# Performance work log

Measured on AMD Instinct MI355X. Metric: run time of the kernel, lower is better.

## Reference

```python
import jax, jax.numpy as jnp
import numpy as np
from math import log2

B, N, H, D, HID, BLK = 4, 4096, 16, 64, 1024, 128
THETA = 10000.0
SCALE = D ** -0.5
ATTN_EPS = 1e-8
LN_EPS = 1e-5


def setup_inputs() -> dict:
    key = jax.random.key(0)
    ks = jax.random.split(key, 3)
    return {
        "hidden_states": jax.random.normal(ks[0], (B, N, HID), jnp.float32),
        "ln_gamma": jnp.ones((HID,), jnp.float32),
        "ln_beta": jnp.zeros((HID,), jnp.float32),
        "w_qkv": jax.random.normal(ks[1], (HID, 3 * H * D), jnp.float32) * 0.02,
        "w_out": jax.random.normal(ks[2], (H * D, HID), jnp.float32) * 0.02,
        "b_out": jnp.zeros((HID,), jnp.float32),
    }


def _rotary_freqs(n):
    # faithful to source: 1.0 / (theta ** arange(0,dim,2) / dim)  (note precedence)
    exps = jnp.arange(0, D, 2, dtype=jnp.float32)[: D // 2]
    inv = 1.0 / (THETA ** exps / D)
    f = jnp.arange(n, dtype=jnp.float32)[:, None] * inv[None, :]  # (n, D/2)
    return jnp.repeat(f, 2, axis=-1)  # (n, D), each freq duplicated pairwise


def _apply_rotary(freqs, t):
    cos, sin = jnp.cos(freqs), jnp.sin(freqs)  # (n, D) broadcast over (bh, n, D)
    x = t.reshape(*t.shape[:-1], D // 2, 2)
    rot = jnp.stack((-x[..., 1], x[..., 0]), axis=-1).reshape(t.shape)
    return t * cos + rot * sin


def _flip_pairs(t):
    # flip every adjacent pair along axis 1
    s = t.shape
    t = t.reshape(s[0], s[1] // 2, 2, *s[2:])
    return t[:, :, ::-1].reshape(s)


def _coarsen(q, k, v):
    pair = lambda t: t.reshape(t.shape[0], -1, 2, D)
    return pair(q).mean(2), pair(k).mean(2), pair(v).sum(2)


def _block_attn(q, k, v):
    # q,k,v: (bh, nblk, z, d); unnormalized softmax numerator + denominator
    S = jnp.einsum('bnid,bnjd->bnij', q, k)
    S = S - S.max(-1, keepdims=True)
    A = jnp.exp(S)
    y = jnp.einsum('bnij,bnjd->bnid', A, v)
    return y.reshape(y.shape[0], -1, D), A.sum(-1).reshape(A.shape[0], -1)


def _forward(hidden_states, ln_gamma, ln_beta, w_qkv, w_out, b_out):
    # LayerNorm
    mu = hidden_states.mean(-1, keepdims=True)
    var = hidden_states.var(-1, keepdims=True)
    x = (hidden_states - mu) / jnp.sqrt(var + LN_EPS) * ln_gamma + ln_beta

    # QKV projection, split heads -> (B*H, N, D)
    qkv = x @ w_qkv
    q, k, v = jnp.split(qkv, 3, axis=-1)
    heads = lambda t: t.reshape(B, N, H, D).transpose(0, 2, 1, 3).reshape(B * H, N, D)
    q, k, v = heads(q), heads(k), heads(v)

    q = q * SCALE
    freqs = _rotary_freqs(N)
    q = _apply_rotary(freqs, q)
    k = _apply_rotary(freqs, k)

    num_levels = int(log2(N // BLK)) - 1
    qkvs = [(q, k, v)]
    for _ in range(num_levels):
        qkvs.append(_coarsen(*qkvs[-1]))
    qkvs = [qkvs[0]] + qkvs  # finest level used twice (near + flipped neighbor)

    Ys = []
    n_lv = len(qkvs)
    for ind, (q_, k_, v_) in enumerate(reversed(qkvs)):
        is_last = ind == n_lv - 1
        tb = lambda t: t.reshape(t.shape[0], -1, BLK, D)
        qb, kb, vb = tb(q_), tb(k_), tb(v_)
        if not is_last:
            kb, vb = _flip_pairs(kb), _flip_pairs(vb)
        Ys.append(_block_attn(qb, kb, vb))

    Y, A = Ys[0]
    for ind in range(1, len(Ys)):
        if ind != len(Ys) - 1:
            Y = jnp.repeat(Y, 2, axis=1)
            A = jnp.repeat(A, 2, axis=1)
        Y = Ys[ind][0] + Y
        A = Ys[ind][1] + A

    out = Y / (A + ATTN_EPS)[..., None]
    out = out.reshape(B, H, N, D).transpose(0, 2, 1, 3).reshape(B, N, H * D)
    return out @ w_out + b_out


def reference(hidden_states, ln_gamma, ln_beta, w_qkv, w_out, b_out):
    return _forward(hidden_states, ln_gamma, ln_beta, w_qkv, w_out, b_out)
```

## Files before the change

kernel.cpp:

```cpp
#include <hip/hip_runtime.h>
#include <math.h>

#define NTOK 4096
#define NB 4
#define NH 16
#define HD 64
#define HID 1024
#define BH 64
#define QSCALE 0.125f

typedef unsigned short u16;
typedef unsigned int u32;
typedef __attribute__((ext_vector_type(8))) _Float16 f16x8;
typedef __attribute__((ext_vector_type(8))) short s16x8;
typedef __attribute__((ext_vector_type(4))) float f32x4;
#define MFMA_F16(a, b, c) __builtin_amdgcn_mfma_f32_16x16x32_f16(a, b, c, 0, 0, 0)
#define MFMA_BF16(a, b, c) __builtin_amdgcn_mfma_f32_16x16x32_bf16(a, b, c, 0, 0, 0)
#define GLDS16(gptr, lptr)                                                          \
  __builtin_amdgcn_global_load_lds(                                                \
      (const __attribute__((address_space(1))) void*)(gptr),                       \
      (__attribute__((address_space(3))) void*)(lptr), 16, 0, 0)
#define VMCNT0() asm volatile("s_waitcnt vmcnt(0)" ::: "memory")
#define VMCNT4() asm volatile("s_waitcnt vmcnt(4)" ::: "memory")
#define SCHED_FENCE() __builtin_amdgcn_sched_barrier(0)

__device__ __forceinline__ float bf2f(u32 u) {
  union { u32 i; float f; } x; x.i = u << 16; return x.f;
}
__device__ __forceinline__ u32 f2bf(float f) {
  union { float f; u32 i; } x; x.f = f;
  return (x.i + 0x7fffu + ((x.i >> 16) & 1u)) >> 16;
}
__device__ __forceinline__ u32 pk2(float a, float b) {
  return f2bf(a) | (f2bf(b) << 16);
}
__device__ __forceinline__ u32 pkh2(float a, float b) {
  _Float16 ha = (_Float16)a, hb = (_Float16)b;
  u16 x, y;
  __builtin_memcpy(&x, &ha, 2);
  __builtin_memcpy(&y, &hb, 2);
  return (u32)x | ((u32)y << 16);
}
__device__ __forceinline__ u16 f2h(float a) {
  _Float16 h = (_Float16)a;
  u16 x;
  __builtin_memcpy(&x, &h, 2);
  return x;
}
__device__ __forceinline__ void up8(uint4 a, float* f) {
  f[0] = bf2f(a.x & 0xffffu); f[1] = bf2f(a.x >> 16);
  f[2] = bf2f(a.y & 0xffffu); f[3] = bf2f(a.y >> 16);
  f[4] = bf2f(a.z & 0xffffu); f[5] = bf2f(a.z >> 16);
  f[6] = bf2f(a.w & 0xffffu); f[7] = bf2f(a.w >> 16);
}
__device__ __forceinline__ void up8h(uint4 a, float* f) {
  union { uint4 u; _Float16 h[8]; } x;
  x.u = a;
#pragma unroll
  for (int c = 0; c < 8; ++c) f[c] = (float)x.h[c];
}

__global__ void fill_kernel(float* __restrict__ out, int n, float v) {
  int i = blockIdx.x * 256 + threadIdx.x;
  if (i < n) out[i] = v;
}

__global__ void rope_table_kernel(float* __restrict__ ct, float* __restrict__ st) {
  int idx = blockIdx.x * 256 + threadIdx.x;
  if (idx >= NTOK * 32) return;
  int n = idx >> 5, i = idx & 31;
  float t = powf(10000.0f, (float)(2 * i));
  float inv = 1.0f / (t / 64.0f);
  float f = (float)n * inv;
  ct[idx] = cosf(f);
  st[idx] = sinf(f);
}

__global__ __launch_bounds__(256) void ln_f16_kernel(const float* __restrict__ in,
                                                     const float* __restrict__ gm,
                                                     const float* __restrict__ bt,
                                                     u16* __restrict__ out) {
  __shared__ float sh[8];
  int row = blockIdx.x, t = threadIdx.x;
  float4 x = ((const float4*)(in + (size_t)row * HID))[t];
  float s1 = x.x + x.y + x.z + x.w;
  float s2 = x.x * x.x + x.y * x.y + x.z * x.z + x.w * x.w;
#pragma unroll
  for (int o = 32; o > 0; o >>= 1) {
    s1 += __shfl_down(s1, o, 64);
    s2 += __shfl_down(s2, o, 64);
  }
  if ((t & 63) == 0) { sh[t >> 6] = s1; sh[4 + (t >> 6)] = s2; }
  __syncthreads();
  float S1 = sh[0] + sh[1] + sh[2] + sh[3];
  float S2 = sh[4] + sh[5] + sh[6] + sh[7];
  float mu = S1 * (1.0f / HID);
  float var = S2 * (1.0f / HID) - mu * mu;
  float rstd = 1.0f / sqrtf(var + 1e-5f);
  float4 g = ((const float4*)gm)[t], b = ((const float4*)bt)[t];
  float o0 = (x.x - mu) * rstd * g.x + b.x;
  float o1 = (x.y - mu) * rstd * g.y + b.y;
  float o2 = (x.z - mu) * rstd * g.z + b.z;
  float o3 = (x.w - mu) * rstd * g.w + b.w;
  *(uint2*)&out[(size_t)row * HID + t * 4] = make_uint2(pkh2(o0, o1), pkh2(o2, o3));
}

__global__ __launch_bounds__(256) void prep_w_kernel(const float* __restrict__ w,
                                                     u16* __restrict__ wt, int N) {
  __shared__ float T[64][65];
  int t = threadIdx.x;
  int n0 = blockIdx.x * 64, k0 = blockIdx.y * 64;
  {
    int k = t >> 2, nc = (t & 3) * 16;
    const float* src = w + (size_t)(k0 + k) * N + n0 + nc;
#pragma unroll
    for (int i = 0; i < 4; ++i) {
      float4 x = *(const float4*)(src + i * 4);
      T[nc + i * 4 + 0][k] = x.x;
      T[nc + i * 4 + 1][k] = x.y;
      T[nc + i * 4 + 2][k] = x.z;
      T[nc + i * 4 + 3][k] = x.w;
    }
  }
  __syncthreads();
  {
    int n = t >> 2, kc = (t & 3) * 16;
    u32 pk[8];
#pragma unroll
    for (int j = 0; j < 8; ++j) pk[j] = pkh2(T[n][kc + 2 * j], T[n][kc + 2 * j + 1]);
    size_t dst = (size_t)(n0 + n) * 1024 + k0 + kc;
    *(uint4*)&wt[dst] = make_uint4(pk[0], pk[1], pk[2], pk[3]);
    *(uint4*)&wt[dst + 8] = make_uint4(pk[4], pk[5], pk[6], pk[7]);
  }
}

template <int MODE>
__global__ __launch_bounds__(256) void gemm_f16_kernel(
    const u16* __restrict__ At, const u16* __restrict__ Bt,
    u16* __restrict__ qd, u16* __restrict__ kd, u16* __restrict__ vd,
    const float* __restrict__ ct, const float* __restrict__ st,
    const float* __restrict__ bias, float* __restrict__ C, int nxb) {
  constexpr int BUF = 128 * 32;
  __shared__ __align__(16) u16 As[3 * BUF], Bs[3 * BUF];
  const int t = threadIdx.x;
  const int nwg = gridDim.x;
  const int bid = blockIdx.x;
  const int wid = (bid & 7) * (nwg >> 3) + (bid >> 3);
  const int m0 = (wid / nxb) * 128, n0 = (wid % nxb) * 128;
  const int l = t & 63, w = t >> 6;
  const int wm = w & 1, wn = w >> 1;
  const int lr = l & 15;
  const int kgs = (((l >> 4) ^ ((lr >> 1) & 3))) * 8;

  const int schunk = (l & 3) ^ ((l >> 3) & 3);
  const u16* gA = At + (size_t)(m0 + w * 32 + (l >> 2)) * 1024 + schunk * 8;
  const u16* gB = Bt + (size_t)(n0 + w * 32 + (l >> 2)) * 1024 + schunk * 8;
  const int wbase = (w * 32) * 32;

  f32x4 zero4 = {0.f, 0.f, 0.f, 0.f};
  f32x4 acc[4][4];
#pragma unroll
  for (int mf = 0; mf < 4; ++mf)
#pragma unroll
    for (int nf = 0; nf < 4; ++nf) acc[mf][nf] = zero4;

  GLDS16(gA, &As[wbase]);
  GLDS16(gA + (size_t)16 * 1024, &As[wbase + 16 * 32]);
  GLDS16(gB, &Bs[wbase]);
  GLDS16(gB + (size_t)16 * 1024, &Bs[wbase + 16 * 32]);
  GLDS16(gA + 32, &As[BUF + wbase]);
  GLDS16(gA + 32 + (size_t)16 * 1024, &As[BUF + wbase + 16 * 32]);
  GLDS16(gB + 32, &Bs[BUF + wbase]);
  GLDS16(gB + 32 + (size_t)16 * 1024, &Bs[BUF + wbase + 16 * 32]);
  VMCNT4();
  __builtin_amdgcn_s_barrier();
  SCHED_FENCE();

  int cur = 0;
  for (int step = 0; step < 32; ++step) {
    int nx2 = cur + 2; if (nx2 >= 3) nx2 -= 3;
    if (step + 2 < 32) {
      int k2 = (step + 2) * 32;
      GLDS16(gA + k2, &As[nx2 * BUF + wbase]);
      GLDS16(gA + k2 + (size_t)16 * 1024, &As[nx2 * BUF + wbase + 16 * 32]);
      GLDS16(gB + k2, &Bs[nx2 * BUF + wbase]);
      GLDS16(gB + k2 + (size_t)16 * 1024, &Bs[nx2 * BUF + wbase + 16 * 32]);
    }
    {
      const int cb = cur * BUF;
      f16x8 af[4];
#pragma unroll
      for (int mf = 0; mf < 4; ++mf)
        af[mf] = *(const f16x8*)&As[cb + (wm * 64 + mf * 16 + lr) * 32 + kgs];
#pragma unroll
      for (int nf = 0; nf < 4; ++nf) {
        f16x8 bf = *(const f16x8*)&Bs[cb + (wn * 64 + nf * 16 + lr) * 32 + kgs];
#pragma unroll
        for (int mf = 0; mf < 4; ++mf) acc[mf][nf] = MFMA_F16(af[mf], bf, acc[mf][nf]);
      }
    }
    if (step + 1 < 32) {
      SCHED_FENCE();
      if (step + 2 < 32) VMCNT4();
      else               VMCNT0();
      __builtin_amdgcn_s_barrier();
      SCHED_FENCE();
    }
    cur = cur + 1; if (cur >= 3) cur -= 3;
  }

  if (MODE == 0) {
#pragma unroll
    for (int nf = 0; nf < 4; ++nf) {
      int col = n0 + wn * 64 + nf * 16 + (l & 15);
      int which = col >> 10;
      int rem = col & 1023;
      int h = rem >> 6, d = rem & 63;
      int fi = d >> 1;
      float sc = (which == 0) ? QSCALE : 1.0f;
#pragma unroll
      for (int mf = 0; mf < 4; ++mf) {
#pragma unroll
        for (int r = 0; r < 4; ++r) {
          int row = m0 + wm * 64 + mf * 16 + (l >> 4) * 4 + r;
          int bbo = row >> 12, n = row & 4095;
          size_t idx = ((size_t)(bbo * NH + h) * NTOK + n) * HD + d;
          float val = acc[mf][nf][r];
          if (which == 2) {
            vd[idx] = f2h(val);
          } else {
            float par = __shfl_xor(val, 1);
            float cc = ct[n * 32 + fi], ss = st[n * 32 + fi];
            float a0 = val * sc, a1 = par * sc;
            float o = (d & 1) ? fmaf(a0, cc, a1 * ss) : fmaf(a0, cc, -(a1 * ss));
            ((which == 0) ? qd : kd)[idx] = (u16)f2bf(o);
          }
        }
      }
    }
  } else {
#pragma unroll
    for (int nf = 0; nf < 4; ++nf) {
      int col = n0 + wn * 64 + nf * 16 + (l & 15);
      float bl_ = bias[col];
#pragma unroll
      for (int mf = 0; mf < 4; ++mf) {
#pragma unroll
        for (int r = 0; r < 4; ++r) {
          int row = m0 + wm * 64 + mf * 16 + (l >> 4) * 4 + r;
          C[(size_t)row * 1024 + col] = acc[mf][nf][r] + bl_;
        }
      }
    }
  }
}

#define KP 72
#define VP 136
#define PP 136
template <int LV, int FINE>
__global__ __launch_bounds__(256, 2) void attn_mfma_kernel(
    const u16* __restrict__ qg, const u16* __restrict__ kgl, const u16* __restrict__ vg,
    float* __restrict__ yl, float* __restrict__ al) {
  constexpr int R = 1 << LV;
  constexpr float QKSC = 1.0f / (float)R;
  __shared__ __align__(16) u16 Ks[128 * KP];
  __shared__ __align__(16) u16 Vt[64 * VP];
  __shared__ __align__(16) u16 Ps[128 * PP];
  const int t = threadIdx.x;
  const int blk = blockIdx.x, bh = blockIdx.y;
  const int l = t & 63, w = t >> 6;
  const int lr = l & 15, lg = l >> 4;
  const int nl = NTOK >> LV;
  const size_t bbase = (size_t)bh * NTOK;

  s16x8 aq[2][2];
#pragma unroll
  for (int mf = 0; mf < 2; ++mf)
#pragma unroll
    for (int ks = 0; ks < 2; ++ks) {
      int qrow = blk * 128 + w * 32 + mf * 16 + lr;
      const u16* src = qg + (bbase + ((size_t)qrow << LV)) * HD + ks * 32 + lg * 8;
      if (LV == 0) {
        aq[mf][ks] = *(const s16x8*)src;
      } else {
        float s[8] = {};
#pragma unroll
        for (int ss = 0; ss < R; ++ss) {
          uint4 a = *(const uint4*)(src + (size_t)ss * HD);
          float f[8];
          up8(a, f);
#pragma unroll
          for (int c = 0; c < 8; ++c) s[c] += f[c];
        }
        union { uint4 u; s16x8 v; } cv;
        cv.u = make_uint4(pk2(s[0] * QKSC, s[1] * QKSC), pk2(s[2] * QKSC, s[3] * QKSC),
                          pk2(s[4] * QKSC, s[5] * QKSC), pk2(s[6] * QKSC, s[7] * QKSC));
        aq[mf][ks] = cv.v;
      }
    }

  f32x4 zero4 = {0.f, 0.f, 0.f, 0.f};
  f32x4 accY[2][4];
  float asum[2][4];
#pragma unroll
  for (int mf = 0; mf < 2; ++mf)
#pragma unroll
    for (int nf = 0; nf < 4; ++nf) accY[mf][nf] = zero4;
#pragma unroll
  for (int mf = 0; mf < 2; ++mf)
#pragma unroll
    for (int r = 0; r < 4; ++r) asum[mf][r] = 0.f;

  const int npass = FINE ? 2 : 1;
  for (int pass = 0; pass < npass; ++pass) {
    const int kblk = (pass == 0) ? (blk ^ 1) : blk;
    __syncthreads();
#pragma unroll
    for (int it = 0; it < 2; ++it) {
      int kk = it * 64 + (t >> 2), dq = (t & 3) * 16;
      const u16* src = kgl + (bbase + (((size_t)kblk * 128 + kk) << LV)) * HD + dq;
      if (LV == 0) {
        *(uint4*)&Ks[kk * KP + dq] = *(const uint4*)src;
        *(uint4*)&Ks[kk * KP + dq + 8] = *(const uint4*)(src + 8);
      } else {
        float s[16] = {};
#pragma unroll
        for (int ss = 0; ss < R; ++ss) {
          float f[8];
          up8(*(const uint4*)(src + (size_t)ss * HD), f);
#pragma unroll
          for (int c = 0; c < 8; ++c) s[c] += f[c];
          up8(*(const uint4*)(src + (size_t)ss * HD + 8), f);
#pragma unroll
          for (int c = 0; c < 8; ++c) s[8 + c] += f[c];
        }
        u32 pk[8];
#pragma unroll
        for (int j = 0; j < 8; ++j) pk[j] = pk2(s[2 * j] * QKSC, s[2 * j + 1] * QKSC);
        *(uint4*)&Ks[kk * KP + dq] = make_uint4(pk[0], pk[1], pk[2], pk[3]);
        *(uint4*)&Ks[kk * KP + dq + 8] = make_uint4(pk[4], pk[5], pk[6], pk[7]);
      }
    }
#pragma unroll
    for (int it = 0; it < 2; ++it) {
      int kk = it * 64 + (t >> 2), dq = (t & 3) * 16;
      const u16* src = vg + (bbase + (((size_t)kblk * 128 + kk) << LV)) * HD + dq;
      u16 hv[16];
      if (LV == 0) {
        union { uint4 u; u16 h[8]; } a0, a1;
        a0.u = *(const uint4*)src;
        a1.u = *(const uint4*)(src + 8);
#pragma unroll
        for (int c = 0; c < 8; ++c) { hv[c] = a0.h[c]; hv[8 + c] = a1.h[c]; }
      } else {
        float s[16] = {};
#pragma unroll
        for (int ss = 0; ss < R; ++ss) {
          float f[8];
          up8h(*(const uint4*)(src + (size_t)ss * HD), f);
#pragma unroll
          for (int c = 0; c < 8; ++c) s[c] += f[c];
          up8h(*(const uint4*)(src + (size_t)ss * HD + 8), f);
#pragma unroll
          for (int c = 0; c < 8; ++c) s[8 + c] += f[c];
        }
#pragma unroll
        for (int c = 0; c < 16; ++c) hv[c] = f2h(s[c]);
      }
#pragma unroll
      for (int c = 0; c < 16; ++c) {
        int dv = dq + c;
        int col = kk ^ (((dv >> 4) & 1) << 5) ^ (((dv >> 5) & 1) << 3);
        Vt[dv * VP + col] = hv[c];
      }
    }
    __syncthreads();
    f32x4 accS[2][8];
#pragma unroll
    for (int mf = 0; mf < 2; ++mf)
#pragma unroll
      for (int nf = 0; nf < 8; ++nf) accS[mf][nf] = zero4;
#pragma unroll
    for (int nf = 0; nf < 8; ++nf)
#pragma unroll
      for (int ks = 0; ks < 2; ++ks) {
        s16x8 bk = *(const s16x8*)&Ks[(nf * 16 + lr) * KP + ks * 32 + lg * 8];
        accS[0][nf] = MFMA_BF16(aq[0][ks], bk, accS[0][nf]);
        accS[1][nf] = MFMA_BF16(aq[1][ks], bk, accS[1][nf]);
      }
#pragma unroll
    for (int mf = 0; mf < 2; ++mf)
#pragma unroll
      for (int r = 0; r < 4; ++r) {
        float m = accS[mf][0][r];
#pragma unroll
        for (int nf = 1; nf < 8; ++nf) m = fmaxf(m, accS[mf][nf][r]);
#pragma unroll
        for (int xm = 1; xm < 16; xm <<= 1) m = fmaxf(m, __shfl_xor(m, xm));
        float s = 0.f;
#pragma unroll
        for (int nf = 0; nf < 8; ++nf) {
          float e = __expf(accS[mf][nf][r] - m);
          accS[mf][nf][r] = e;
          s += e;
        }
#pragma unroll
        for (int xm = 1; xm < 16; xm <<= 1) s += __shfl_xor(s, xm);
        asum[mf][r] += s;
      }
#pragma unroll
    for (int mf = 0; mf < 2; ++mf)
#pragma unroll
      for (int nf = 0; nf < 8; ++nf)
#pragma unroll
        for (int r = 0; r < 4; ++r) {
          int qrow = w * 32 + mf * 16 + lg * 4 + r;
          int col = (nf * 16 + lr) ^ (((qrow >> 3) & 1) << 4);
          Ps[qrow * PP + col] = f2h(accS[mf][nf][r]);
        }
    __syncthreads();
#pragma unroll
    for (int ks4 = 0; ks4 < 4; ++ks4) {
      f16x8 ap[2];
#pragma unroll
      for (int mf = 0; mf < 2; ++mf) {
        int prow = w * 32 + mf * 16 + lr;
        int koff = (ks4 * 32 + lg * 8) ^ (((lr >> 3) & 1) << 4);
        ap[mf] = *(const f16x8*)&Ps[prow * PP + koff];
      }
#pragma unroll
      for (int nf = 0; nf < 4; ++nf) {
        int koff = (ks4 * 32 + lg * 8) ^ ((nf & 1) << 5) ^ (((nf >> 1) & 1) << 3);
        f16x8 bv = *(const f16x8*)&Vt[(nf * 16 + lr) * VP + koff];
        accY[0][nf] = MFMA_F16(ap[0], bv, accY[0][nf]);
        accY[1][nf] = MFMA_F16(ap[1], bv, accY[1][nf]);
      }
    }
  }
#pragma unroll
  for (int mf = 0; mf < 2; ++mf) {
    if (lr == 0) {
#pragma unroll
      for (int r = 0; r < 4; ++r)
        al[(size_t)bh * nl + blk * 128 + w * 32 + mf * 16 + lg * 4 + r] = asum[mf][r];
    }
#pragma unroll
    for (int nf = 0; nf < 4; ++nf)
#pragma unroll
      for (int r = 0; r < 4; ++r) {
        int qrow = blk * 128 + w * 32 + mf * 16 + lg * 4 + r;
        yl[((size_t)bh * nl + qrow) * HD + nf * 16 + lr] = accY[mf][nf][r];
      }
  }
}

__global__ __launch_bounds__(256) void combine_pyr_kernel(
    const float* __restrict__ Yf, const float* __restrict__ Y1, const float* __restrict__ Y2,
    const float* __restrict__ Y3, const float* __restrict__ Y4,
    const float* __restrict__ Af, const float* __restrict__ A1, const float* __restrict__ A2,
    const float* __restrict__ A3, const float* __restrict__ A4, u16* __restrict__ out) {
  int row = blockIdx.x, t = threadIdx.x;
  int b = row >> 12, tok = row & 4095;
  int h = t >> 4, d = (t & 15) * 4;
  int bh = b * NH + h;
  float a = Af[(size_t)bh * 4096 + tok] + A1[(size_t)bh * 2048 + (tok >> 1)] +
            A2[(size_t)bh * 1024 + (tok >> 2)] + A3[(size_t)bh * 512 + (tok >> 3)] +
            A4[(size_t)bh * 256 + (tok >> 4)] + 1e-8f;
  float4 y0 = *(const float4*)&Yf[((size_t)bh * 4096 + tok) * HD + d];
  float4 y1 = *(const float4*)&Y1[((size_t)bh * 2048 + (tok >> 1)) * HD + d];
  float4 y2 = *(const float4*)&Y2[((size_t)bh * 1024 + (tok >> 2)) * HD + d];
  float4 y3 = *(const float4*)&Y3[((size_t)bh * 512 + (tok >> 3)) * HD + d];
  float4 y4 = *(const float4*)&Y4[((size_t)bh * 256 + (tok >> 4)) * HD + d];
  float inv = 1.0f / a;
  float o0 = (y0.x + y1.x + y2.x + y3.x + y4.x) * inv;
  float o1 = (y0.y + y1.y + y2.y + y3.y + y4.y) * inv;
  float o2 = (y0.z + y1.z + y2.z + y3.z + y4.z) * inv;
  float o3 = (y0.w + y1.w + y2.w + y3.w + y4.w) * inv;
  *(uint2*)&out[(size_t)row * HID + t * 4] = make_uint2(pkh2(o0, o1), pkh2(o2, o3));
}

extern "C" void kernel_launch(void* const* d_in, const int* in_sizes, int n_in,
                              void* d_out, int out_size, void* d_ws, size_t ws_size,
                              hipStream_t stream) {
  (void)in_sizes; (void)n_in;
  const float* hs = (const float*)d_in[0];
  const float* gm = (const float*)d_in[1];
  const float* bt = (const float*)d_in[2];
  const float* wqkv = (const float*)d_in[3];
  const float* wout = (const float*)d_in[4];
  const float* bout = (const float*)d_in[5];
  float* out = (float*)d_out;

  const size_t MB = 1024ull * 1024ull;
  unsigned char* base = (unsigned char*)d_ws;
  const size_t need = 232 * MB;
  if (ws_size < need) {
    fill_kernel<<<(out_size + 255) / 256, 256, 0, stream>>>(out, out_size,
                                                            1000.0f + (float)(ws_size >> 20));
    return;
  }

  u16* Qf = (u16*)(base);
  u16* Kf = (u16*)(base + 32 * MB);
  u16* Vf = (u16*)(base + 64 * MB);
  float* YACC = (float*)(base + 96 * MB);
  float* Y1 = (float*)(base + 160 * MB);
  float* Y2 = (float*)(base + 192 * MB);
  float* Y3 = (float*)(base + 208 * MB);
  float* Y4 = (float*)(base + 216 * MB);
  float* AACC = (float*)(base + 220 * MB);
  float* A1 = AACC + (size_t)BH * 4096;
  float* A2 = A1 + (size_t)BH * 2048;
  float* A3 = A2 + (size_t)BH * 1024;
  float* A4 = A3 + (size_t)BH * 512;
  u16* WQT = (u16*)(base + 223 * MB);
  u16* WOT = (u16*)(base + 229 * MB);
  float* CT = (float*)(base + 231 * MB);
  float* ST = CT + NTOK * 32;
  u16* ALN = (u16*)(base + 96 * MB);
  u16* ATT = (u16*)(base);

  rope_table_kernel<<<(NTOK * 32 + 255) / 256, 256, 0, stream>>>(CT, ST);
  ln_f16_kernel<<<NB * NTOK, 256, 0, stream>>>(hs, gm, bt, ALN);
  prep_w_kernel<<<dim3(48, 16), 256, 0, stream>>>(wqkv, WQT, 3072);
  prep_w_kernel<<<dim3(16, 16), 256, 0, stream>>>(wout, WOT, 1024);

  gemm_f16_kernel<0><<<3072, 256, 0, stream>>>(
      ALN, WQT, Qf, Kf, Vf, CT, ST, nullptr, nullptr, 24);

  attn_mfma_kernel<0, 1><<<dim3(32, BH), 256, 0, stream>>>(Qf, Kf, Vf, YACC, AACC);
  attn_mfma_kernel<1, 0><<<dim3(16, BH), 256, 0, stream>>>(Qf, Kf, Vf, Y1, A1);
  attn_mfma_kernel<2, 0><<<dim3(8, BH), 256, 0, stream>>>(Qf, Kf, Vf, Y2, A2);
  attn_mfma_kernel<3, 0><<<dim3(4, BH), 256, 0, stream>>>(Qf, Kf, Vf, Y3, A3);
  attn_mfma_kernel<4, 0><<<dim3(2, BH), 256, 0, stream>>>(Qf, Kf, Vf, Y4, A4);

  combine_pyr_kernel<<<NB * NTOK, 256, 0, stream>>>(YACC, Y1, Y2, Y3, Y4,
                                                    AACC, A1, A2, A3, A4, ATT);
  gemm_f16_kernel<1><<<1024, 256, 0, stream>>>(
      ATT, WOT, nullptr, nullptr, nullptr, nullptr, nullptr, bout, out, 8);
}
```

Before: 561.8 us.

## Pre-transpose V, compute transposed attention tiles, store partial outputs in fp16

Adds a kernel that transposes V into a d-major layout so the attention kernels load V rows directly into shared memory with vector loads. This replaces the scalar swizzled per-element transpose done in each block. The QK and PV MFMAs now run with swapped operands, producing S^T and Y^T. That lets softmax reductions use two cross-lane shuffles and lets P be written with packed stores without a barrier. Per-level partial outputs are stored as fp16 instead of fp32, halving combine traffic at some precision cost, and the extra transpose kernel adds one pass over V.

```diff
diff --git a/kernel.cpp b/kernel.cpp
--- a/kernel.cpp
+++ b/kernel.cpp
@@ -59,6 +59,12 @@
 #pragma unroll
   for (int c = 0; c < 8; ++c) f[c] = (float)x.h[c];
 }
+__device__ __forceinline__ void up4h(uint2 a, float* f) {
+  union { uint2 u; _Float16 h[4]; } x;
+  x.u = a;
+#pragma unroll
+  for (int c = 0; c < 4; ++c) f[c] = (float)x.h[c];
+}
 
 __global__ void fill_kernel(float* __restrict__ out, int n, float v) {
   int i = blockIdx.x * 256 + threadIdx.x;
@@ -131,6 +137,29 @@
     size_t dst = (size_t)(n0 + n) * 1024 + k0 + kc;
     *(uint4*)&wt[dst] = make_uint4(pk[0], pk[1], pk[2], pk[3]);
     *(uint4*)&wt[dst + 8] = make_uint4(pk[4], pk[5], pk[6], pk[7]);
+  }
+}
+
+__global__ __launch_bounds__(256) void transpose_v_kernel(const u16* __restrict__ vf,
+                                                          u16* __restrict__ vt) {
+  __shared__ u16 T[64][72];
+  int bh = blockIdx.y, tok0 = blockIdx.x * 64;
+  int t = threadIdx.x;
+  {
+    int tk = t >> 2, d0 = (t & 3) * 16;
+    const u16* src = vf + ((size_t)bh * NTOK + tok0 + tk) * HD + d0;
+    *(uint4*)&T[tk][d0] = *(const uint4*)src;
+    *(uint4*)&T[tk][d0 + 8] = *(const uint4*)(src + 8);
+  }
+  __syncthreads();
+  {
+    int dv = t >> 2, k0 = (t & 3) * 16;
+    union { u16 v[16]; uint4 q[2]; } o;
+#pragma unroll
+    for (int i = 0; i < 16; ++i) o.v[i] = T[k0 + i][dv];
+    u16* dst = vt + ((size_t)bh * HD + dv) * NTOK + tok0 + k0;
+    *(uint4*)dst = o.q[0];
+    *(uint4*)(dst + 8) = o.q[1];
   }
 }
 
@@ -260,8 +289,8 @@
 #define PP 136
 template <int LV, int FINE>
 __global__ __launch_bounds__(256, 2) void attn_mfma_kernel(
-    const u16* __restrict__ qg, const u16* __restrict__ kgl, const u16* __restrict__ vg,
-    float* __restrict__ yl, float* __restrict__ al) {
+    const u16* __restrict__ qg, const u16* __restrict__ kgl, const u16* __restrict__ vtg,
+    u16* __restrict__ yl, float* __restrict__ al) {
   constexpr int R = 1 << LV;
   constexpr float QKSC = 1.0f / (float)R;
   __shared__ __align__(16) u16 Ks[128 * KP];
@@ -276,13 +305,13 @@
 
   s16x8 aq[2][2];
 #pragma unroll
-  for (int mf = 0; mf < 2; ++mf)
+  for (int qf = 0; qf < 2; ++qf)
 #pragma unroll
     for (int ks = 0; ks < 2; ++ks) {
-      int qrow = blk * 128 + w * 32 + mf * 16 + lr;
+      int qrow = blk * 128 + w * 32 + qf * 16 + lr;
       const u16* src = qg + (bbase + ((size_t)qrow << LV)) * HD + ks * 32 + lg * 8;
       if (LV == 0) {
-        aq[mf][ks] = *(const s16x8*)src;
+        aq[qf][ks] = *(const s16x8*)src;
       } else {
         float s[8] = {};
 #pragma unroll
@@ -296,21 +325,17 @@
         union { uint4 u; s16x8 v; } cv;
         cv.u = make_uint4(pk2(s[0] * QKSC, s[1] * QKSC), pk2(s[2] * QKSC, s[3] * QKSC),
                           pk2(s[4] * QKSC, s[5] * QKSC), pk2(s[6] * QKSC, s[7] * QKSC));
-        aq[mf][ks] = cv.v;
+        aq[qf][ks] = cv.v;
       }
     }
 
   f32x4 zero4 = {0.f, 0.f, 0.f, 0.f};
-  f32x4 accY[2][4];
-  float asum[2][4];
-#pragma unroll
-  for (int mf = 0; mf < 2; ++mf)
-#pragma unroll
-    for (int nf = 0; nf < 4; ++nf) accY[mf][nf] = zero4;
-#pragma unroll
-  for (int mf = 0; mf < 2; ++mf)
-#pragma unroll
-    for (int r = 0; r < 4; ++r) asum[mf][r] = 0.f;
+  f32x4 accYT[4][2];
+  float asum[2] = {0.f, 0.f};
+#pragma unroll
+  for (int dvf = 0; dvf < 4; ++dvf)
+#pragma unroll
+    for (int qf = 0; qf < 2; ++qf) accYT[dvf][qf] = zero4;
 
   const int npass = FINE ? 2 : 1;
   for (int pass = 0; pass < npass; ++pass) {
@@ -342,122 +367,112 @@
         *(uint4*)&Ks[kk * KP + dq + 8] = make_uint4(pk[4], pk[5], pk[6], pk[7]);
       }
     }
-#pragma unroll
-    for (int it = 0; it < 2; ++it) {
-      int kk = it * 64 + (t >> 2), dq = (t & 3) * 16;
-      const u16* src = vg + (bbase + (((size_t)kblk * 128 + kk) << LV)) * HD + dq;
-      u16 hv[16];
+    {
+      int dv = t >> 2, j0 = (t & 3) * 32;
+      const u16* src = vtg + ((size_t)bh * HD + dv) * NTOK +
+                       (((size_t)(kblk * 128 + j0)) << LV);
       if (LV == 0) {
-        union { uint4 u; u16 h[8]; } a0, a1;
-        a0.u = *(const uint4*)src;
-        a1.u = *(const uint4*)(src + 8);
-#pragma unroll
-        for (int c = 0; c < 8; ++c) { hv[c] = a0.h[c]; hv[8 + c] = a1.h[c]; }
+#pragma unroll
+        for (int c = 0; c < 4; ++c)
+          *(uint4*)&Vt[dv * VP + j0 + c * 8] = *(const uint4*)(src + c * 8);
       } else {
-        float s[16] = {};
-#pragma unroll
-        for (int ss = 0; ss < R; ++ss) {
+        float acc[32];
+#pragma unroll
+        for (int j = 0; j < 32; ++j) acc[j] = 0.f;
+#pragma unroll
+        for (int c = 0; c < 4 * R; ++c) {
           float f[8];
-          up8h(*(const uint4*)(src + (size_t)ss * HD), f);
-#pragma unroll
-          for (int c = 0; c < 8; ++c) s[c] += f[c];
-          up8h(*(const uint4*)(src + (size_t)ss * HD + 8), f);
-#pragma unroll
-          for (int c = 0; c < 8; ++c) s[8 + c] += f[c];
-        }
-#pragma unroll
-        for (int c = 0; c < 16; ++c) hv[c] = f2h(s[c]);
-      }
-#pragma unroll
-      for (int c = 0; c < 16; ++c) {
-        int dv = dq + c;
-        int col = kk ^ (((dv >> 4) & 1) << 5) ^ (((dv >> 5) & 1) << 3);
-        Vt[dv * VP + col] = hv[c];
+          up8h(*(const uint4*)(src + c * 8), f);
+#pragma unroll
+          for (int e = 0; e < 8; ++e) acc[(c * 8 + e) >> LV] += f[e];
+        }
+#pragma unroll
+        for (int j = 0; j < 32; j += 8) {
+          uint4 pkv;
+          pkv.x = pkh2(acc[j + 0], acc[j + 1]);
+          pkv.y = pkh2(acc[j + 2], acc[j + 3]);
+          pkv.z = pkh2(acc[j + 4], acc[j + 5]);
+          pkv.w = pkh2(acc[j + 6], acc[j + 7]);
+          *(uint4*)&Vt[dv * VP + j0 + j] = pkv;
+        }
       }
     }
     __syncthreads();
-    f32x4 accS[2][8];
-#pragma unroll
-    for (int mf = 0; mf < 2; ++mf)
-#pragma unroll
-      for (int nf = 0; nf < 8; ++nf) accS[mf][nf] = zero4;
-#pragma unroll
-    for (int nf = 0; nf < 8; ++nf)
+    f32x4 accST[8][2];
+#pragma unroll
+    for (int kf = 0; kf < 8; ++kf)
+#pragma unroll
+      for (int qf = 0; qf < 2; ++qf) accST[kf][qf] = zero4;
+#pragma unroll
+    for (int kf = 0; kf < 8; ++kf)
 #pragma unroll
       for (int ks = 0; ks < 2; ++ks) {
-        s16x8 bk = *(const s16x8*)&Ks[(nf * 16 + lr) * KP + ks * 32 + lg * 8];
-        accS[0][nf] = MFMA_BF16(aq[0][ks], bk, accS[0][nf]);
-        accS[1][nf] = MFMA_BF16(aq[1][ks], bk, accS[1][nf]);
-      }
-#pragma unroll
-    for (int mf = 0; mf < 2; ++mf)
-#pragma unroll
-      for (int r = 0; r < 4; ++r) {
-        float m = accS[mf][0][r];
-#pragma unroll
-        for (int nf = 1; nf < 8; ++nf) m = fmaxf(m, accS[mf][nf][r]);
-#pragma unroll
-        for (int xm = 1; xm < 16; xm <<= 1) m = fmaxf(m, __shfl_xor(m, xm));
-        float s = 0.f;
-#pragma unroll
-        for (int nf = 0; nf < 8; ++nf) {
-          float e = __expf(accS[mf][nf][r] - m);
-          accS[mf][nf][r] = e;
+        s16x8 ak = *(const s16x8*)&Ks[(kf * 16 + lr) * KP + ks * 32 + lg * 8];
+        accST[kf][0] = MFMA_BF16(ak, aq[0][ks], accST[kf][0]);
+        accST[kf][1] = MFMA_BF16(ak, aq[1][ks], accST[kf][1]);
+      }
+#pragma unroll
+    for (int qf = 0; qf < 2; ++qf) {
+      float m = accST[0][qf][0];
+#pragma unroll
+      for (int kf = 0; kf < 8; ++kf)
+#pragma unroll
+        for (int r = 0; r < 4; ++r) m = fmaxf(m, accST[kf][qf][r]);
+      m = fmaxf(m, __shfl_xor(m, 16));
+      m = fmaxf(m, __shfl_xor(m, 32));
+      float s = 0.f;
+#pragma unroll
+      for (int kf = 0; kf < 8; ++kf) {
+#pragma unroll
+        for (int r = 0; r < 4; ++r) {
+          float e = __expf(accST[kf][qf][r] - m);
+          accST[kf][qf][r] = e;
           s += e;
         }
-#pragma unroll
-        for (int xm = 1; xm < 16; xm <<= 1) s += __shfl_xor(s, xm);
-        asum[mf][r] += s;
-      }
-#pragma unroll
-    for (int mf = 0; mf < 2; ++mf)
-#pragma unroll
-      for (int nf = 0; nf < 8; ++nf)
-#pragma unroll
-        for (int r = 0; r < 4; ++r) {
-          int qrow = w * 32 + mf * 16 + lg * 4 + r;
-          int col = (nf * 16 + lr) ^ (((qrow >> 3) & 1) << 4);
-          Ps[qrow * PP + col] = f2h(accS[mf][nf][r]);
-        }
-    __syncthreads();
+      }
+      s += __shfl_xor(s, 16);
+      s += __shfl_xor(s, 32);
+      asum[qf] += s;
+#pragma unroll
+      for (int kf = 0; kf < 8; ++kf) {
+        uint2 pw;
+        pw.x = pkh2(accST[kf][qf][0], accST[kf][qf][1]);
+        pw.y = pkh2(accST[kf][qf][2], accST[kf][qf][3]);
+        *(uint2*)&Ps[(w * 32 + qf * 16 + lr) * PP + kf * 16 + lg * 4] = pw;
+      }
+    }
 #pragma unroll
     for (int ks4 = 0; ks4 < 4; ++ks4) {
-      f16x8 ap[2];
-#pragma unroll
-      for (int mf = 0; mf < 2; ++mf) {
-        int prow = w * 32 + mf * 16 + lr;
-        int koff = (ks4 * 32 + lg * 8) ^ (((lr >> 3) & 1) << 4);
-        ap[mf] = *(const f16x8*)&Ps[prow * PP + koff];
-      }
-#pragma unroll
-      for (int nf = 0; nf < 4; ++nf) {
-        int koff = (ks4 * 32 + lg * 8) ^ ((nf & 1) << 5) ^ (((nf >> 1) & 1) << 3);
-        f16x8 bv = *(const f16x8*)&Vt[(nf * 16 + lr) * VP + koff];
-        accY[0][nf] = MFMA_F16(ap[0], bv, accY[0][nf]);
-        accY[1][nf] = MFMA_F16(ap[1], bv, accY[1][nf]);
-      }
-    }
-  }
-#pragma unroll
-  for (int mf = 0; mf < 2; ++mf) {
-    if (lr == 0) {
-#pragma unroll
-      for (int r = 0; r < 4; ++r)
-        al[(size_t)bh * nl + blk * 128 + w * 32 + mf * 16 + lg * 4 + r] = asum[mf][r];
-    }
-#pragma unroll
-    for (int nf = 0; nf < 4; ++nf)
-#pragma unroll
-      for (int r = 0; r < 4; ++r) {
-        int qrow = blk * 128 + w * 32 + mf * 16 + lg * 4 + r;
-        yl[((size_t)bh * nl + qrow) * HD + nf * 16 + lr] = accY[mf][nf][r];
-      }
+      f16x8 pf[2];
+#pragma unroll
+      for (int qf = 0; qf < 2; ++qf)
+        pf[qf] = *(const f16x8*)&Ps[(w * 32 + qf * 16 + lr) * PP + ks4 * 32 + lg * 8];
+#pragma unroll
+      for (int dvf = 0; dvf < 4; ++dvf) {
+        f16x8 vf = *(const f16x8*)&Vt[(dvf * 16 + lr) * VP + ks4 * 32 + lg * 8];
+        accYT[dvf][0] = MFMA_F16(vf, pf[0], accYT[dvf][0]);
+        accYT[dvf][1] = MFMA_F16(vf, pf[1], accYT[dvf][1]);
+      }
+    }
+  }
+#pragma unroll
+  for (int qf = 0; qf < 2; ++qf) {
+    if (lg == 0)
+      al[(size_t)bh * nl + blk * 128 + w * 32 + qf * 16 + lr] = asum[qf];
+    int q = blk * 128 + w * 32 + qf * 16 + lr;
+#pragma unroll
+    for (int dvf = 0; dvf < 4; ++dvf) {
+      uint2 yw;
+      yw.x = pkh2(accYT[dvf][qf][0], accYT[dvf][qf][1]);
+      yw.y = pkh2(accYT[dvf][qf][2], accYT[dvf][qf][3]);
+      *(uint2*)&yl[((size_t)bh * nl + q) * HD + dvf * 16 + lg * 4] = yw;
+    }
   }
 }
 
 __global__ __launch_bounds__(256) void combine_pyr_kernel(
-    const float* __restrict__ Yf, const float* __restrict__ Y1, const float* __restrict__ Y2,
-    const float* __restrict__ Y3, const float* __restrict__ Y4,
+    const u16* __restrict__ Yf, const u16* __restrict__ Y1, const u16* __restrict__ Y2,
+    const u16* __restrict__ Y3, const u16* __restrict__ Y4,
     const float* __restrict__ Af, const float* __restrict__ A1, const float* __restrict__ A2,
     const float* __restrict__ A3, const float* __restrict__ A4, u16* __restrict__ out) {
   int row = blockIdx.x, t = threadIdx.x;
@@ -467,17 +482,25 @@
   float a = Af[(size_t)bh * 4096 + tok] + A1[(size_t)bh * 2048 + (tok >> 1)] +
             A2[(size_t)bh * 1024 + (tok >> 2)] + A3[(size_t)bh * 512 + (tok >> 3)] +
             A4[(size_t)bh * 256 + (tok >> 4)] + 1e-8f;
-  float4 y0 = *(const float4*)&Yf[((size_t)bh * 4096 + tok) * HD + d];
-  float4 y1 = *(const float4*)&Y1[((size_t)bh * 2048 + (tok >> 1)) * HD + d];
-  float4 y2 = *(const float4*)&Y2[((size_t)bh * 1024 + (tok >> 2)) * HD + d];
-  float4 y3 = *(const float4*)&Y3[((size_t)bh * 512 + (tok >> 3)) * HD + d];
-  float4 y4 = *(const float4*)&Y4[((size_t)bh * 256 + (tok >> 4)) * HD + d];
+  float y[4] = {0.f, 0.f, 0.f, 0.f}, f[4];
+  up4h(*(const uint2*)&Yf[((size_t)bh * 4096 + tok) * HD + d], f);
+#pragma unroll
+  for (int c = 0; c < 4; ++c) y[c] += f[c];
+  up4h(*(const uint2*)&Y1[((size_t)bh * 2048 + (tok >> 1)) * HD + d], f);
+#pragma unroll
+  for (int c = 0; c < 4; ++c) y[c] += f[c];
+  up4h(*(const uint2*)&Y2[((size_t)bh * 1024 + (tok >> 2)) * HD + d], f);
+#pragma unroll
+  for (int c = 0; c < 4; ++c) y[c] += f[c];
+  up4h(*(const uint2*)&Y3[((size_t)bh * 512 + (tok >> 3)) * HD + d], f);
+#pragma unroll
+  for (int c = 0; c < 4; ++c) y[c] += f[c];
+  up4h(*(const uint2*)&Y4[((size_t)bh * 256 + (tok >> 4)) * HD + d], f);
+#pragma unroll
+  for (int c = 0; c < 4; ++c) y[c] += f[c];
   float inv = 1.0f / a;
-  float o0 = (y0.x + y1.x + y2.x + y3.x + y4.x) * inv;
-  float o1 = (y0.y + y1.y + y2.y + y3.y + y4.y) * inv;
-  float o2 = (y0.z + y1.z + y2.z + y3.z + y4.z) * inv;
-  float o3 = (y0.w + y1.w + y2.w + y3.w + y4.w) * inv;
-  *(uint2*)&out[(size_t)row * HID + t * 4] = make_uint2(pkh2(o0, o1), pkh2(o2, o3));
+  *(uint2*)&out[(size_t)row * HID + t * 4] =
+      make_uint2(pkh2(y[0] * inv, y[1] * inv), pkh2(y[2] * inv, y[3] * inv));
 }
 
 extern "C" void kernel_launch(void* const* d_in, const int* in_sizes, int n_in,
@@ -494,7 +517,7 @@
 
   const size_t MB = 1024ull * 1024ull;
   unsigned char* base = (unsigned char*)d_ws;
-  const size_t need = 232 * MB;
+  const size_t need = 233 * MB;
   if (ws_size < need) {
     fill_kernel<<<(out_size + 255) / 256, 256, 0, stream>>>(out, out_size,
                                                             1000.0f + (float)(ws_size >> 20));
@@ -504,21 +527,22 @@
   u16* Qf = (u16*)(base);
   u16* Kf = (u16*)(base + 32 * MB);
   u16* Vf = (u16*)(base + 64 * MB);
-  float* YACC = (float*)(base + 96 * MB);
-  float* Y1 = (float*)(base + 160 * MB);
-  float* Y2 = (float*)(base + 192 * MB);
-  float* Y3 = (float*)(base + 208 * MB);
-  float* Y4 = (float*)(base + 216 * MB);
-  float* AACC = (float*)(base + 220 * MB);
+  u16* Yf = (u16*)(base + 96 * MB);
+  u16* VT = (u16*)(base + 128 * MB);
+  u16* Y1 = (u16*)(base + 160 * MB);
+  u16* Y2 = (u16*)(base + 176 * MB);
+  u16* Y3 = (u16*)(base + 184 * MB);
+  u16* Y4 = (u16*)(base + 188 * MB);
+  float* AACC = (float*)(base + 190 * MB);
   float* A1 = AACC + (size_t)BH * 4096;
   float* A2 = A1 + (size_t)BH * 2048;
   float* A3 = A2 + (size_t)BH * 1024;
   float* A4 = A3 + (size_t)BH * 512;
-  u16* WQT = (u16*)(base + 223 * MB);
-  u16* WOT = (u16*)(base + 229 * MB);
-  float* CT = (float*)(base + 231 * MB);
+  u16* WQT = (u16*)(base + 192 * MB);
+  u16* WOT = (u16*)(base + 198 * MB);
+  float* CT = (float*)(base + 200 * MB);
   float* ST = CT + NTOK * 32;
-  u16* ALN = (u16*)(base + 96 * MB);
+  u16* ALN = (u16*)(base + 201 * MB);
   u16* ATT = (u16*)(base);
 
   rope_table_kernel<<<(NTOK * 32 + 255) / 256, 256, 0, stream>>>(CT, ST);
@@ -528,14 +552,15 @@
 
   gemm_f16_kernel<0><<<3072, 256, 0, stream>>>(
       ALN, WQT, Qf, Kf, Vf, CT, ST, nullptr, nullptr, 24);
-
-  attn_mfma_kernel<0, 1><<<dim3(32, BH), 256, 0, stream>>>(Qf, Kf, Vf, YACC, AACC);
-  attn_mfma_kernel<1, 0><<<dim3(16, BH), 256, 0, stream>>>(Qf, Kf, Vf, Y1, A1);
-  attn_mfma_kernel<2, 0><<<dim3(8, BH), 256, 0, stream>>>(Qf, Kf, Vf, Y2, A2);
-  attn_mfma_kernel<3, 0><<<dim3(4, BH), 256, 0, stream>>>(Qf, Kf, Vf, Y3, A3);
-  attn_mfma_kernel<4, 0><<<dim3(2, BH), 256, 0, stream>>>(Qf, Kf, Vf, Y4, A4);
-
-  combine_pyr_kernel<<<NB * NTOK, 256, 0, stream>>>(YACC, Y1, Y2, Y3, Y4,
+  transpose_v_kernel<<<dim3(NTOK / 64, BH), 256, 0, stream>>>(Vf, VT);
+
+  attn_mfma_kernel<0, 1><<<dim3(32, BH), 256, 0, stream>>>(Qf, Kf, VT, Yf, AACC);
+  attn_mfma_kernel<1, 0><<<dim3(16, BH), 256, 0, stream>>>(Qf, Kf, VT, Y1, A1);
+  attn_mfma_kernel<2, 0><<<dim3(8, BH), 256, 0, stream>>>(Qf, Kf, VT, Y2, A2);
+  attn_mfma_kernel<3, 0><<<dim3(4, BH), 256, 0, stream>>>(Qf, Kf, VT, Y3, A3);
+  attn_mfma_kernel<4, 0><<<dim3(2, BH), 256, 0, stream>>>(Qf, Kf, VT, Y4, A4);
+
+  combine_pyr_kernel<<<NB * NTOK, 256, 0, stream>>>(Yf, Y1, Y2, Y3, Y4,
                                                     AACC, A1, A2, A3, A4, ATT);
   gemm_f16_kernel<1><<<1024, 256, 0, stream>>>(
       ATT, WOT, nullptr, nullptr, nullptr, nullptr, nullptr, bout, out, 8);
```

Result: faster. 540.1 us (-3.9%).
